# Kernel optimization log

Measured on AMD Instinct MI355X. Metric: run time of the kernel, lower is better.

Reference implementation:

```python
import jax, jax.numpy as jnp
import numpy as np

N_NODES = 100000
N_EDGES = 3200000
D_IN = 128
D_HID = 128
N_CLASSES = 2
N_GRAPHS = 64


def _gcn_conv(x, src, dst, norm, W, b, n_nodes):
    # GCNConv: x' = D^-1/2 (A+I) D^-1/2 (x W) + b  (self-loops already in src/dst)
    h = x @ W                                   # [N, out]
    msg = h[src] * norm[:, None]                # gather + per-edge scale [E', out]
    agg = jax.ops.segment_sum(msg, dst, num_segments=n_nodes)  # scatter-add
    return agg + b


def setup_inputs() -> dict:
    key = jax.random.key(0)
    ks = jax.random.split(key, 10)
    x = jax.random.normal(ks[0], (N_NODES, D_IN), dtype=jnp.float32)
    edge_index = jax.random.randint(ks[1], (2, N_EDGES), 0, N_NODES, dtype=jnp.int32)
    batch = jnp.sort(jax.random.randint(ks[2], (N_NODES,), 0, N_GRAPHS, dtype=jnp.int32))
    s1 = 1.0 / np.sqrt(D_IN)
    s2 = 1.0 / np.sqrt(D_HID)
    W1 = jax.random.uniform(ks[3], (D_IN, D_HID), jnp.float32, -s1, s1)
    b1 = jnp.zeros((D_HID,), jnp.float32)
    W2 = jax.random.uniform(ks[4], (D_HID, D_HID), jnp.float32, -s2, s2)
    b2 = jnp.zeros((D_HID,), jnp.float32)
    Wc = jax.random.uniform(ks[5], (D_HID, N_CLASSES), jnp.float32, -s2, s2)
    bc = jnp.zeros((N_CLASSES,), jnp.float32)
    return {"x": x, "edge_index": edge_index, "batch": batch,
            "W1": W1, "b1": b1, "W2": W2, "b2": b2, "Wc": Wc, "bc": bc,
            "num_graphs": N_GRAPHS}


def reference(x, edge_index, batch, W1, b1, W2, b2, Wc, bc, num_graphs):
    n = x.shape[0]
    loops = jnp.arange(n, dtype=edge_index.dtype)
    src = jnp.concatenate([edge_index[0], loops])
    dst = jnp.concatenate([edge_index[1], loops])
    # symmetric normalization with self-loops (degree over destinations, as PyG)
    deg = jax.ops.segment_sum(jnp.ones_like(dst, dtype=x.dtype), dst, num_segments=n)
    dinv = jnp.where(deg > 0, jax.lax.rsqrt(jnp.maximum(deg, 1.0)), 0.0)
    norm = dinv[src] * dinv[dst]                # [E']

    h = _gcn_conv(x, src, dst, norm, W1, b1, n)
    h = jax.nn.relu(h)                          # dropout is identity at eval
    h = _gcn_conv(h, src, dst, norm, W2, b2, n)

    # global_mean_pool over graph ids
    sums = jax.ops.segment_sum(h, batch, num_segments=num_graphs)      # [G, H]
    cnts = jax.ops.segment_sum(jnp.ones((n,), h.dtype), batch, num_segments=num_graphs)
    pooled = sums / jnp.maximum(cnts, 1.0)[:, None]

    return pooled @ Wc + bc                     # [G, num_classes]
```

## Files before the change

kernel.cpp:

```cpp
#include <hip/hip_runtime.h>
#include <hip/hip_bf16.h>

#define D 128
#define NGRAPH 64
#define POOLBLK 256
#define PBCHUNK 4096
#define WINSZ 256
#define WINSLOTS 16384
#define XP 136

typedef __attribute__((ext_vector_type(4))) float f32x4;
typedef __attribute__((ext_vector_type(8))) short bf16x8;

__device__ __forceinline__ unsigned short f2bf(float f) {
    union { float f; unsigned int i; } u; u.f = f;
    unsigned int r = u.i + 0x7fffu + ((u.i >> 16) & 1u);
    return (unsigned short)(r >> 16);
}
__device__ __forceinline__ float2 bf2_to_f2(unsigned int u) {
    union { unsigned int i; float f; } a, b;
    a.i = u << 16;
    b.i = u & 0xffff0000u;
    return make_float2(a.f, b.f);
}


__global__ __launch_bounds__(256) void k_part(const int* __restrict__ src,
                                              const int* __restrict__ dst,
                                              int* __restrict__ cursor,
                                              unsigned* __restrict__ ebuf,
                                              const float* __restrict__ W2,
                                              const float* __restrict__ Wc,
                                              const float* __restrict__ b2,
                                              const float* __restrict__ bc,
                                              float* __restrict__ Weff,
                                              float* __restrict__ beff,
                                              int E, int nb) {
    __shared__ unsigned spack[PBCHUNK];
    __shared__ unsigned short sbin[PBCHUNK];
    __shared__ unsigned short slrank[PBCHUNK];
    __shared__ int hist[400];
    __shared__ int base[400];
    int tid = threadIdx.x;
    for (int i = tid; i < nb; i += 256) hist[i] = 0;
    __syncthreads();
    int b0 = blockIdx.x * PBCHUNK;
    int cnt = min(PBCHUNK, E - b0);
    for (int j = tid; j < cnt; j += 256) {
        int s = __builtin_nontemporal_load(&src[b0 + j]);
        int d = __builtin_nontemporal_load(&dst[b0 + j]);
        int bin = d >> 8;
        spack[j] = (unsigned)s | ((unsigned)(d & 255) << 17);
        sbin[j] = (unsigned short)bin;
        slrank[j] = (unsigned short)atomicAdd(&hist[bin], 1);
    }
    __syncthreads();
    for (int i = tid; i < nb; i += 256)
        base[i] = hist[i] ? atomicAdd(&cursor[i], hist[i]) : 0;
    __syncthreads();
    for (int j = tid; j < cnt; j += 256) {
        int bin = sbin[j];
        ebuf[(size_t)bin * WINSLOTS + base[bin] + slrank[j]] = spack[j];
    }
    if (blockIdx.x == 0) {
        int i = tid >> 1, c = tid & 1;
        float acc = 0.f;
        for (int k = 0; k < D; ++k) acc += W2[i * D + k] * Wc[k * 2 + c];
        Weff[i * 2 + c] = acc;
        if (i == 0) {
            float s = 0.f;
            for (int k = 0; k < D; ++k) s += b2[k] * Wc[k * 2 + c];
            beff[c] = s + bc[c];
        }
    }
}

__global__ __launch_bounds__(256) void k_csrwin(const unsigned* __restrict__ ebuf,
                                                const int* __restrict__ cursor,
                                                int* __restrict__ csr,
                                                int2* __restrict__ offcnt,
                                                float* __restrict__ dinv, int n) {
    __shared__ int hist[WINSZ];
    __shared__ int lscan[WINSZ];
    __shared__ int sexcl[WINSZ];
    int b = blockIdx.x;
    int tid = threadIdx.x;
    hist[tid] = 0;
    __syncthreads();
    int cnt = cursor[b];
    const unsigned* eb = ebuf + (size_t)b * WINSLOTS;
    for (int j = tid; j < cnt; j += 256)
        atomicAdd(&hist[eb[j] >> 17], 1);
    __syncthreads();
    int deg = hist[tid];
    lscan[tid] = deg;
    __syncthreads();
    for (int off = 1; off < 256; off <<= 1) {
        int y = (tid >= off) ? lscan[tid - off] : 0;
        __syncthreads();
        lscan[tid] += y;
        __syncthreads();
    }
    int excl = lscan[tid] - deg;
    int v = b * WINSZ + tid;
    int gbase = b * WINSLOTS;
    if (v < n) {
        offcnt[v] = make_int2(gbase + excl, deg);
        dinv[v] = rsqrtf((float)(deg + 1));
    }
    hist[tid] = 0;
    sexcl[tid] = excl;
    __syncthreads();
    for (int j = tid; j < cnt; j += 256) {
        unsigned p = eb[j];
        int d8 = (int)(p >> 17);
        int lr = atomicAdd(&hist[d8], 1);
        csr[gbase + sexcl[d8] + lr] = (int)(p & 0x1FFFFu);
    }
}


__global__ __launch_bounds__(256) void k_gemm_mfma(const float* __restrict__ X,
                                                   const float* __restrict__ W1,
                                                   const float* __restrict__ dinv,
                                                   unsigned short* __restrict__ H, int nrows) {
    __shared__ unsigned short xs[64][XP];
    __shared__ unsigned short wt[128][XP];
    int tid = threadIdx.x;
    int m0 = blockIdx.x * 64;
    for (int i = tid; i < 2048; i += 256) {
        int elt = i * 8;
        int k = elt >> 7, n0 = elt & 127;
        float4 a = *(const float4*)&W1[k * D + n0];
        float4 b = *(const float4*)&W1[k * D + n0 + 4];
        wt[n0 + 0][k] = f2bf(a.x); wt[n0 + 1][k] = f2bf(a.y);
        wt[n0 + 2][k] = f2bf(a.z); wt[n0 + 3][k] = f2bf(a.w);
        wt[n0 + 4][k] = f2bf(b.x); wt[n0 + 5][k] = f2bf(b.y);
        wt[n0 + 6][k] = f2bf(b.z); wt[n0 + 7][k] = f2bf(b.w);
    }
    for (int i = tid; i < 2048; i += 256) {
        int elt = i * 4;
        int r = elt >> 7, c = elt & 127;
        int gr = m0 + r;
        float4 v = (gr < nrows) ? *(const float4*)&X[(size_t)gr * D + c]
                                : make_float4(0.f, 0.f, 0.f, 0.f);
        ushort4 bv;
        bv.x = f2bf(v.x); bv.y = f2bf(v.y); bv.z = f2bf(v.z); bv.w = f2bf(v.w);
        *(ushort4*)&xs[r][c] = bv;
    }
    __syncthreads();
    int wv = tid >> 6, lane = tid & 63;
    int lrow = lane & 15, lk = (lane >> 4) * 8;
    f32x4 acc[8];
#pragma unroll
    for (int i = 0; i < 8; ++i) acc[i] = (f32x4){0.f, 0.f, 0.f, 0.f};
#pragma unroll
    for (int kk = 0; kk < 128; kk += 32) {
        bf16x8 a = *(bf16x8*)&xs[wv * 16 + lrow][kk + lk];
#pragma unroll
        for (int nt = 0; nt < 8; ++nt) {
            bf16x8 b = *(bf16x8*)&wt[nt * 16 + lrow][kk + lk];
            acc[nt] = __builtin_amdgcn_mfma_f32_16x16x32_bf16(a, b, acc[nt], 0, 0, 0);
        }
    }
    int orow = m0 + wv * 16 + (lane >> 4) * 4;
    float dvr[4];
#pragma unroll
    for (int r = 0; r < 4; ++r) dvr[r] = (orow + r < nrows) ? dinv[orow + r] : 0.f;
#pragma unroll
    for (int nt = 0; nt < 8; ++nt) {
#pragma unroll
        for (int r = 0; r < 4; ++r) {
            int gr = orow + r;
            if (gr < nrows) H[(size_t)gr * D + nt * 16 + lrow] = f2bf(acc[nt][r] * dvr[r]);
        }
    }
}


__global__ __launch_bounds__(256) void k_agg_proj(const unsigned short* __restrict__ H,
                                                  const int2* __restrict__ offcnt,
                                                  const int* __restrict__ csr,
                                                  const float* __restrict__ dinv,
                                                  const float* __restrict__ bias,
                                                  const float* __restrict__ Weff,
                                                  float2* __restrict__ z, int n) {
    int wid = threadIdx.x >> 6;
    int lane = threadIdx.x & 63;
    int v = blockIdx.x * 4 + wid;
    if (v >= n) return;
    float dv = dinv[v];
    int l2 = lane * 2;
    unsigned us = *(const unsigned*)(H + (size_t)v * D + l2);
    float2 hs = bf2_to_f2(us);
    float2 acc = make_float2(hs.x, hs.y);
    int2 oc = offcnt[v];
    int e = oc.x, eE = oc.x + oc.y;
    for (; e + 15 < eE; e += 16) {
        int s[16];
#pragma unroll
        for (int j = 0; j < 16; ++j) s[j] = csr[e + j];
        unsigned u[16];
#pragma unroll
        for (int j = 0; j < 16; ++j) u[j] = *(const unsigned*)(H + (size_t)s[j] * D + l2);
#pragma unroll
        for (int j = 0; j < 16; ++j) {
            float2 h = bf2_to_f2(u[j]);
            acc.x += h.x; acc.y += h.y;
        }
    }
    for (; e + 7 < eE; e += 8) {
        int s[8];
#pragma unroll
        for (int j = 0; j < 8; ++j) s[j] = csr[e + j];
        unsigned u[8];
#pragma unroll
        for (int j = 0; j < 8; ++j) u[j] = *(const unsigned*)(H + (size_t)s[j] * D + l2);
#pragma unroll
        for (int j = 0; j < 8; ++j) {
            float2 h = bf2_to_f2(u[j]);
            acc.x += h.x; acc.y += h.y;
        }
    }
    for (; e + 3 < eE; e += 4) {
        int s0 = csr[e], s1 = csr[e + 1], s2 = csr[e + 2], s3 = csr[e + 3];
        unsigned u0 = *(const unsigned*)(H + (size_t)s0 * D + l2);
        unsigned u1 = *(const unsigned*)(H + (size_t)s1 * D + l2);
        unsigned u2 = *(const unsigned*)(H + (size_t)s2 * D + l2);
        unsigned u3 = *(const unsigned*)(H + (size_t)s3 * D + l2);
        float2 h0 = bf2_to_f2(u0), h1 = bf2_to_f2(u1);
        float2 h2 = bf2_to_f2(u2), h3 = bf2_to_f2(u3);
        acc.x += h0.x + h1.x + h2.x + h3.x;
        acc.y += h0.y + h1.y + h2.y + h3.y;
    }
    for (; e < eE; ++e) {
        int s0 = csr[e];
        unsigned u0 = *(const unsigned*)(H + (size_t)s0 * D + l2);
        float2 h0 = bf2_to_f2(u0);
        acc.x += h0.x; acc.y += h0.y;
    }
    float2 b = ((const float2*)bias)[lane];
    acc.x = fmaxf(acc.x * dv + b.x, 0.f);
    acc.y = fmaxf(acc.y * dv + b.y, 0.f);
    float4 wv = *(const float4*)&Weff[l2 * 2];
    float z0 = acc.x * wv.x + acc.y * wv.z;
    float z1 = acc.x * wv.y + acc.y * wv.w;
#pragma unroll
    for (int off = 32; off >= 1; off >>= 1) {
        z0 += __shfl_xor(z0, off, 64);
        z1 += __shfl_xor(z1, off, 64);
    }
    if (lane == 0) z[v] = make_float2(z0, z1);
}


__global__ __launch_bounds__(256) void k_pool_edges(const float2* __restrict__ z,
                                                    const int* __restrict__ src,
                                                    const int* __restrict__ dst,
                                                    const float* __restrict__ dinv,
                                                    const int* __restrict__ batch,
                                                    float* __restrict__ tsum,
                                                    int* __restrict__ cnt,
                                                    int n, int E) {
    __shared__ float t[4][NGRAPH * 2];
    __shared__ int scnt[4][NGRAPH];
    int tid = threadIdx.x;
    int wv = tid >> 6;
    for (int j = tid; j < 4 * NGRAPH * 2; j += 256) ((float*)t)[j] = 0.f;
    for (int j = tid; j < 4 * NGRAPH; j += 256) ((int*)scnt)[j] = 0;
    __syncthreads();

    int i = (blockIdx.x * 256 + tid) * 4;
    int stride = POOLBLK * 256 * 4;
    for (; i < E; i += stride) {
        if (i + 3 < E) {
            int4 s4 = *(const int4*)&src[i];
            int4 d4 = *(const int4*)&dst[i];
            float w0 = dinv[s4.x] * dinv[d4.x];
            float w1 = dinv[s4.y] * dinv[d4.y];
            float w2 = dinv[s4.z] * dinv[d4.z];
            float w3 = dinv[s4.w] * dinv[d4.w];
            float2 z0 = z[s4.x], z1 = z[s4.y], z2 = z[s4.z], z3 = z[s4.w];
            int g0 = batch[d4.x], g1 = batch[d4.y], g2 = batch[d4.z], g3 = batch[d4.w];
            atomicAdd(&t[wv][g0 * 2],     w0 * z0.x);
            atomicAdd(&t[wv][g0 * 2 + 1], w0 * z0.y);
            atomicAdd(&t[wv][g1 * 2],     w1 * z1.x);
            atomicAdd(&t[wv][g1 * 2 + 1], w1 * z1.y);
            atomicAdd(&t[wv][g2 * 2],     w2 * z2.x);
            atomicAdd(&t[wv][g2 * 2 + 1], w2 * z2.y);
            atomicAdd(&t[wv][g3 * 2],     w3 * z3.x);
            atomicAdd(&t[wv][g3 * 2 + 1], w3 * z3.y);
        } else {
            for (int j = i; j < E; ++j) {
                int s = src[j], d = dst[j];
                float w = dinv[s] * dinv[d];
                float2 zv = z[s];
                int g = batch[d];
                atomicAdd(&t[wv][g * 2],     w * zv.x);
                atomicAdd(&t[wv][g * 2 + 1], w * zv.y);
            }
        }
    }
    for (int v = blockIdx.x * 256 + tid; v < n; v += POOLBLK * 256) {
        float dv = dinv[v];
        float2 zv = z[v];
        int g = batch[v];
        float w = dv * dv;
        atomicAdd(&t[wv][g * 2],     w * zv.x);
        atomicAdd(&t[wv][g * 2 + 1], w * zv.y);
        atomicAdd(&scnt[wv][g], 1);
    }
    __syncthreads();
    if (tid < NGRAPH * 2) {
        float s = t[0][tid] + t[1][tid] + t[2][tid] + t[3][tid];
        if (s != 0.f) atomicAdd(&tsum[tid], s);
    }
    if (tid < NGRAPH) {
        int s = scnt[0][tid] + scnt[1][tid] + scnt[2][tid] + scnt[3][tid];
        if (s) atomicAdd(&cnt[tid], s);
    }
}

__global__ void k_classify(const float* __restrict__ tsum, const int* __restrict__ cnt,
                           const float* __restrict__ beff, const float* __restrict__ bc,
                           float* __restrict__ out) {
    int t = threadIdx.x;
    if (t >= NGRAPH * 2) return;
    int g = t >> 1, c = t & 1;
    int cg = cnt[g];
    out[t] = cg ? (tsum[t] / (float)cg + beff[c]) : bc[c];
}


extern "C" void kernel_launch(void* const* d_in, const int* in_sizes, int n_in,
                              void* d_out, int out_size, void* d_ws, size_t ws_size,
                              hipStream_t stream) {
    const float* x    = (const float*)d_in[0];
    const int*   ei   = (const int*)d_in[1];
    const int*   batch= (const int*)d_in[2];
    const float* W1   = (const float*)d_in[3];
    const float* b1   = (const float*)d_in[4];
    const float* W2   = (const float*)d_in[5];
    const float* b2   = (const float*)d_in[6];
    const float* Wc   = (const float*)d_in[7];
    const float* bc   = (const float*)d_in[8];

    const int n = in_sizes[0] / D;
    const int E = in_sizes[1] / 2;
    const int* src = ei;
    const int* dst = ei + E;
    const int nb = (n + WINSZ - 1) / WINSZ;

    char* ws = (char*)d_ws;
    size_t off = 0;
    auto carve = [&](size_t bytes) -> char* {
        char* p = ws + off;
        off = (off + bytes + 255) & ~(size_t)255;
        return p;
    };
    unsigned short* bufBF = (unsigned short*)carve((size_t)n * D * 2);
    float2* z     = (float2*)carve((size_t)n * 8);
    unsigned* ebuf= (unsigned*)carve((size_t)nb * WINSLOTS * 4);
    int*   csr    = (int*)  carve((size_t)nb * WINSLOTS * 4);
    const int zero_words = 512 + NGRAPH * 2 + NGRAPH;
    int*   cursor = (int*)  carve(zero_words * 4);
    float* tsum   = (float*)(cursor + 512);
    int*   cnt    = (int*)  (tsum + NGRAPH * 2);
    int2*  offcnt = (int2*) carve((size_t)n * 8);
    float* dinv   = (float*)carve((size_t)n * 4);
    float* Weff   = (float*)carve(D * 2 * 4);
    float* beff   = (float*)carve(2 * 4);

    hipMemsetAsync(cursor, 0, zero_words * 4, stream);

    k_part<<<(E + PBCHUNK - 1) / PBCHUNK, 256, 0, stream>>>(src, dst, cursor, ebuf,
                                                            W2, Wc, b2, bc, Weff, beff, E, nb);
    k_csrwin<<<nb, 256, 0, stream>>>(ebuf, cursor, csr, offcnt, dinv, n);

    k_gemm_mfma<<<(n + 63) / 64, 256, 0, stream>>>(x, W1, dinv, bufBF, n);
    k_agg_proj<<<(n + 3) / 4, 256, 0, stream>>>(bufBF, offcnt, csr, dinv, b1, Weff, z, n);

    k_pool_edges<<<POOLBLK, 256, 0, stream>>>(z, src, dst, dinv, batch, tsum, cnt, n, E);
    k_classify<<<1, 128, 0, stream>>>(tsum, cnt, beff, bc, (float*)d_out);
}
```

Measured before the change: 293.8 us.

## Stage CSR window edges in LDS and load GEMM A operand directly

The CSR window-build kernel now caches up to 12288 packed edges in shared memory during the histogram pass, so the scatter pass reads them from LDS instead of re-reading global memory. The GEMM kernel drops its X staging tile and loads each lane's A fragment straight from global memory, converting to bf16 in registers. The pool block size is also raised to 512. The large LDS stage (48KB) may reduce occupancy of the CSR kernel, and the direct X loads are less coalesced than the staged path.

```diff
diff --git a/kernel.cpp b/kernel.cpp
--- a/kernel.cpp
+++ b/kernel.cpp
@@ -3,10 +3,11 @@
 
 #define D 128
 #define NGRAPH 64
-#define POOLBLK 256
+#define POOLBLK 512
 #define PBCHUNK 4096
 #define WINSZ 256
 #define WINSLOTS 16384
+#define CSTAGE 12288
 #define XP 136
 
 typedef __attribute__((ext_vector_type(4))) float f32x4;
@@ -83,14 +84,19 @@
     __shared__ int hist[WINSZ];
     __shared__ int lscan[WINSZ];
     __shared__ int sexcl[WINSZ];
+    __shared__ unsigned sstage[CSTAGE];
     int b = blockIdx.x;
     int tid = threadIdx.x;
     hist[tid] = 0;
     __syncthreads();
     int cnt = cursor[b];
+    int stcnt = min(cnt, CSTAGE);
     const unsigned* eb = ebuf + (size_t)b * WINSLOTS;
-    for (int j = tid; j < cnt; j += 256)
-        atomicAdd(&hist[eb[j] >> 17], 1);
+    for (int j = tid; j < cnt; j += 256) {
+        unsigned p = eb[j];
+        if (j < CSTAGE) sstage[j] = p;
+        atomicAdd(&hist[p >> 17], 1);
+    }
     __syncthreads();
     int deg = hist[tid];
     lscan[tid] = deg;
@@ -111,7 +117,13 @@
     hist[tid] = 0;
     sexcl[tid] = excl;
     __syncthreads();
-    for (int j = tid; j < cnt; j += 256) {
+    for (int j = tid; j < stcnt; j += 256) {
+        unsigned p = sstage[j];
+        int d8 = (int)(p >> 17);
+        int lr = atomicAdd(&hist[d8], 1);
+        csr[gbase + sexcl[d8] + lr] = (int)(p & 0x1FFFFu);
+    }
+    for (int j = stcnt + tid; j < cnt; j += 256) {
         unsigned p = eb[j];
         int d8 = (int)(p >> 17);
         int lr = atomicAdd(&hist[d8], 1);
@@ -124,7 +136,6 @@
                                                    const float* __restrict__ W1,
                                                    const float* __restrict__ dinv,
                                                    unsigned short* __restrict__ H, int nrows) {
-    __shared__ unsigned short xs[64][XP];
     __shared__ unsigned short wt[128][XP];
     int tid = threadIdx.x;
     int m0 = blockIdx.x * 64;
@@ -138,25 +149,23 @@
         wt[n0 + 4][k] = f2bf(b.x); wt[n0 + 5][k] = f2bf(b.y);
         wt[n0 + 6][k] = f2bf(b.z); wt[n0 + 7][k] = f2bf(b.w);
     }
-    for (int i = tid; i < 2048; i += 256) {
-        int elt = i * 4;
-        int r = elt >> 7, c = elt & 127;
-        int gr = m0 + r;
-        float4 v = (gr < nrows) ? *(const float4*)&X[(size_t)gr * D + c]
-                                : make_float4(0.f, 0.f, 0.f, 0.f);
-        ushort4 bv;
-        bv.x = f2bf(v.x); bv.y = f2bf(v.y); bv.z = f2bf(v.z); bv.w = f2bf(v.w);
-        *(ushort4*)&xs[r][c] = bv;
-    }
     __syncthreads();
     int wv = tid >> 6, lane = tid & 63;
     int lrow = lane & 15, lk = (lane >> 4) * 8;
+    int arow = m0 + wv * 16 + lrow;
+    const float* xrow = X + (size_t)min(arow, nrows - 1) * D;
     f32x4 acc[8];
 #pragma unroll
     for (int i = 0; i < 8; ++i) acc[i] = (f32x4){0.f, 0.f, 0.f, 0.f};
 #pragma unroll
     for (int kk = 0; kk < 128; kk += 32) {
-        bf16x8 a = *(bf16x8*)&xs[wv * 16 + lrow][kk + lk];
+        float4 a0 = *(const float4*)&xrow[kk + lk];
+        float4 a1 = *(const float4*)&xrow[kk + lk + 4];
+        bf16x8 a;
+        a[0] = (short)f2bf(a0.x); a[1] = (short)f2bf(a0.y);
+        a[2] = (short)f2bf(a0.z); a[3] = (short)f2bf(a0.w);
+        a[4] = (short)f2bf(a1.x); a[5] = (short)f2bf(a1.y);
+        a[6] = (short)f2bf(a1.z); a[7] = (short)f2bf(a1.w);
 #pragma unroll
         for (int nt = 0; nt < 8; ++nt) {
             bf16x8 b = *(bf16x8*)&wt[nt * 16 + lrow][kk + lk];
```

Result: faster. 281.6 us (-4.2%).
